# Performance work log

Measured on AMD Instinct MI355X. Metric: run time of the kernel, lower is better.

The kernel has to match this reference:

```python
import jax, jax.numpy as jnp
import numpy as np

N = 100000          # num nodes
E = 3200000         # num edges
H = 512             # hidden_dim
B = 512             # num graphs (batch.max()+1)
MAX_NODES = 500
TEMPERATURE = 1.0
LN_EPS = 1e-5
COS_EPS = 1e-8


def setup_inputs() -> dict:
    key = jax.random.key(0)
    ks = jax.random.split(key, 12)
    x_ggnn = jax.random.normal(ks[0], (N, H), dtype=jnp.float32)
    x_appnp = jax.random.normal(ks[1], (N, H), dtype=jnp.float32)
    edge_index = jax.random.randint(ks[2], (2, E), 0, N, dtype=jnp.int64)
    batch = jnp.sort(jax.random.randint(ks[3], (N,), 0, B, dtype=jnp.int64))
    gin = H * 2 + 4  # gate input dim = 1028
    def xavier(k, fan_in, fan_out, gain=1.0):
        lim = gain * np.sqrt(6.0 / (fan_in + fan_out))
        return jax.random.uniform(k, (fan_in, fan_out), jnp.float32, -lim, lim)
    W1 = xavier(ks[4], gin, H)
    b1 = jnp.zeros((H,), jnp.float32)
    ln_g = jnp.ones((H,), jnp.float32)
    ln_b = jnp.zeros((H,), jnp.float32)
    W2 = xavier(ks[5], H, H // 2)
    b2 = jnp.zeros((H // 2,), jnp.float32)
    W3 = xavier(ks[6], H // 2, 2, gain=0.1)
    b3 = jnp.zeros((2,), jnp.float32)  # init zeros per module
    return {"x_ggnn": x_ggnn, "x_appnp": x_appnp, "edge_index": edge_index,
            "batch": batch, "W1": W1, "b1": b1, "ln_g": ln_g, "ln_b": ln_b,
            "W2": W2, "b2": b2, "W3": W3, "b3": b3}


def _segment_mean(x, seg, num_seg, counts):
    s = jax.ops.segment_sum(x, seg, num_segments=num_seg)
    return s / counts[:, None]


def reference(x_ggnn, x_appnp, edge_index, batch, W1, b1, ln_g, ln_b, W2, b2, W3, b3):
    ones = jnp.ones((N,), jnp.float32)
    counts = jax.ops.segment_sum(ones, batch, num_segments=B)          # [B] nodes per graph
    safe_counts = jnp.maximum(counts, 1.0)
    # per-graph edge counts (edges with both endpoints in same graph)
    src_g = batch[edge_index[0]]
    dst_g = batch[edge_index[1]]
    same = (src_g == dst_g).astype(jnp.float32)
    n_edges = jax.ops.segment_sum(same, src_g, num_segments=B)          # [B]
    # pooled (segment mean) features
    pooled_ggnn = _segment_mean(x_ggnn, batch, B, safe_counts)          # [B,H]
    pooled_appnp = _segment_mean(x_appnp, batch, B, safe_counts)        # [B,H]
    # complexity features
    n_nodes = counts
    scale = jnp.log(n_nodes + 1.0) / np.log(MAX_NODES + 1.0)
    density = n_edges / (n_nodes * (n_nodes - 1.0) + 1e-8)
    avg_degree = n_edges / (n_nodes + 1e-8)
    avg_degree_norm = jnp.minimum(avg_degree / 10.0, 1.0)
    na = jnp.maximum(jnp.linalg.norm(pooled_ggnn, axis=1), COS_EPS)
    nb = jnp.maximum(jnp.linalg.norm(pooled_appnp, axis=1), COS_EPS)
    cos = jnp.sum(pooled_ggnn * pooled_appnp, axis=1) / (na * nb)
    divergence = (1.0 - cos) / 2.0
    complexity = jnp.stack([scale, density, avg_degree_norm, divergence], axis=1)  # [B,4]
    # gate MLP (dropout inactive at inference)
    g = jnp.concatenate([pooled_ggnn, pooled_appnp, complexity], axis=1)  # [B, 2H+4]
    h = g @ W1 + b1
    mu = jnp.mean(h, axis=-1, keepdims=True)
    var = jnp.mean((h - mu) ** 2, axis=-1, keepdims=True)
    h = (h - mu) / jnp.sqrt(var + LN_EPS) * ln_g + ln_b
    h = jax.nn.relu(h)
    h = jax.nn.relu(h @ W2 + b2)
    raw = h @ W3 + b3                                                    # [B,2]
    weights = jax.nn.softmax(raw / TEMPERATURE, axis=1)
    w_local = weights[:, 0]
    w_global = weights[:, 1]
    x_fused = w_local[batch][:, None] * x_ggnn + w_global[batch][:, None] * x_appnp
    return x_fused
```

## Files before the change

kernel.cpp:

```cpp
#include <hip/hip_runtime.h>
#include <math.h>

#define Nn 100000
#define Ee 3200000
#define Hh 512
#define Bb 512
#define GIN 1028

#define OFF_STARTS 0
#define OFF_NEDGE  4096
#define OFF_WL     8192
#define OFF_WG     10240
#define OFF_G      16384
#define OFF_HPART  (OFF_G + (size_t)Bb*GIN*4)
#define OFF_H      (OFF_HPART + (size_t)4*Bb*Hh*4)
#define OFF_HP2    (OFF_H + (size_t)Bb*Hh*4)

__global__ void k_starts(const int* __restrict__ batch, int* __restrict__ starts) {
    int t = threadIdx.x;
    for (int b = t; b <= Bb; b += blockDim.x) {
        int lo = 0, hi = Nn;
        while (lo < hi) { int mid = (lo + hi) >> 1; if (batch[mid] < b) lo = mid + 1; else hi = mid; }
        starts[b] = lo;
    }
}

__global__ void k_edges(const int* __restrict__ ei, const int* __restrict__ batch,
                        int* __restrict__ nedge) {
    int e = blockIdx.x * blockDim.x + threadIdx.x;
    if (e >= Ee) return;
    int s = ei[e], d = ei[Ee + e];
    int gs = batch[s], gd = batch[d];
    if (gs == gd) atomicAdd(&nedge[gs], 1);
}

__global__ __launch_bounds__(256) void k_pool(const float* __restrict__ xg, const float* __restrict__ xa,
                                              const int* __restrict__ starts, const int* __restrict__ nedge,
                                              float* __restrict__ g) {
    int b = blockIdx.x;
    int s = starts[b], e = starts[b + 1];
    int t = threadIdx.x;
    int arr = t >> 7, c4 = t & 127;
    const float4* base = (const float4*)(arr ? xa : xg);
    float4 acc = {0.f, 0.f, 0.f, 0.f};
    for (int i = s; i < e; ++i) {
        float4 v = base[(size_t)i * 128 + c4];
        acc.x += v.x; acc.y += v.y; acc.z += v.z; acc.w += v.w;
    }
    int cnt = e - s;
    float inv = 1.0f / (float)(cnt < 1 ? 1 : cnt);
    float4 m = {acc.x * inv, acc.y * inv, acc.z * inv, acc.w * inv};
    float* grow = g + (size_t)b * GIN;
    *(float4*)(grow + arr * Hh + c4 * 4) = m;

    __shared__ float4 sa[128];
    if (arr) sa[c4] = m;
    __syncthreads();
    float d3 = 0.f, ng = 0.f, na = 0.f;
    if (!arr) {
        float4 q = sa[c4];
        d3 = m.x * q.x + m.y * q.y + m.z * q.z + m.w * q.w;
        ng = m.x * m.x + m.y * m.y + m.z * m.z + m.w * m.w;
    } else {
        na = m.x * m.x + m.y * m.y + m.z * m.z + m.w * m.w;
    }
    for (int off = 32; off; off >>= 1) {
        d3 += __shfl_down(d3, off);
        ng += __shfl_down(ng, off);
        na += __shfl_down(na, off);
    }
    __shared__ float r[12];
    int wid = t >> 6, lane = t & 63;
    if (lane == 0) { r[wid * 3] = d3; r[wid * 3 + 1] = ng; r[wid * 3 + 2] = na; }
    __syncthreads();
    if (t == 0) {
        float D  = r[0] + r[3] + r[6] + r[9];
        float NG = r[1] + r[4] + r[7] + r[10];
        float NA = r[2] + r[5] + r[8] + r[11];
        float nag = fmaxf(sqrtf(NG), 1e-8f);
        float nab = fmaxf(sqrtf(NA), 1e-8f);
        float cosv = D / (nag * nab);
        float n  = (float)cnt;
        float ne = (float)nedge[b];
        grow[1024] = logf(n + 1.f) / logf(501.f);
        grow[1025] = ne / (n * (n - 1.f) + 1e-8f);
        grow[1026] = fminf(ne / (n + 1e-8f) * 0.1f, 1.f);
        grow[1027] = (1.f - cosv) * 0.5f;
    }
}

__global__ __launch_bounds__(256) void k_g1(const float* __restrict__ g, const float* __restrict__ W1,
                                            float* __restrict__ hp) {
    int tj = threadIdx.x & 15, tb = threadIdx.x >> 4;
    int j0 = blockIdx.x * 64 + tj * 4;
    int b0 = blockIdx.y * 64 + tb * 4;
    int kc = blockIdx.z;
    int k = kc * 257, kend = k + 257;
    const float* g0 = g + (size_t)b0 * GIN;
    const float* g1 = g0 + GIN;
    const float* g2 = g1 + GIN;
    const float* g3 = g2 + GIN;
    float4 a0 = {0,0,0,0}, a1 = a0, a2 = a0, a3 = a0;
    for (; k < kend; ++k) {
        float4 w = *(const float4*)(W1 + (size_t)k * Hh + j0);
        float x0 = g0[k], x1 = g1[k], x2 = g2[k], x3 = g3[k];
        a0.x += x0 * w.x; a0.y += x0 * w.y; a0.z += x0 * w.z; a0.w += x0 * w.w;
        a1.x += x1 * w.x; a1.y += x1 * w.y; a1.z += x1 * w.z; a1.w += x1 * w.w;
        a2.x += x2 * w.x; a2.y += x2 * w.y; a2.z += x2 * w.z; a2.w += x2 * w.w;
        a3.x += x3 * w.x; a3.y += x3 * w.y; a3.z += x3 * w.z; a3.w += x3 * w.w;
    }
    float* o = hp + ((size_t)kc * Bb + b0) * Hh + j0;
    *(float4*)(o)           = a0;
    *(float4*)(o + Hh)      = a1;
    *(float4*)(o + 2 * Hh)  = a2;
    *(float4*)(o + 3 * Hh)  = a3;
}

__global__ __launch_bounds__(128) void k_ln(const float* __restrict__ hp, const float* __restrict__ b1,
                                            const float* __restrict__ lng, const float* __restrict__ lnb,
                                            float* __restrict__ h) {
    int b = blockIdx.x, t = threadIdx.x;
    const float4* p0 = (const float4*)(hp + (size_t)b * Hh);
    const float4* p1 = (const float4*)(hp + ((size_t)Bb + b) * Hh);
    const float4* p2 = (const float4*)(hp + ((size_t)2 * Bb + b) * Hh);
    const float4* p3 = (const float4*)(hp + ((size_t)3 * Bb + b) * Hh);
    float4 v0 = p0[t], v1 = p1[t], v2 = p2[t], v3 = p3[t], bb = ((const float4*)b1)[t];
    float4 v = {v0.x + v1.x + v2.x + v3.x + bb.x,
                v0.y + v1.y + v2.y + v3.y + bb.y,
                v0.z + v1.z + v2.z + v3.z + bb.z,
                v0.w + v1.w + v2.w + v3.w + bb.w};
    float s  = v.x + v.y + v.z + v.w;
    float ss = v.x * v.x + v.y * v.y + v.z * v.z + v.w * v.w;
    for (int off = 32; off; off >>= 1) { s += __shfl_down(s, off); ss += __shfl_down(ss, off); }
    __shared__ float sh[4];
    __shared__ float mus, rs;
    int wid = t >> 6, lane = t & 63;
    if (lane == 0) { sh[wid * 2] = s; sh[wid * 2 + 1] = ss; }
    __syncthreads();
    if (t == 0) {
        float S = sh[0] + sh[2], SS = sh[1] + sh[3];
        float mu = S * (1.f / 512.f);
        float var = SS * (1.f / 512.f) - mu * mu;
        mus = mu; rs = rsqrtf(var + 1e-5f);
    }
    __syncthreads();
    float mu = mus, rstd = rs;
    float4 gg = ((const float4*)lng)[t], be = ((const float4*)lnb)[t];
    float4 o;
    o.x = fmaxf((v.x - mu) * rstd * gg.x + be.x, 0.f);
    o.y = fmaxf((v.y - mu) * rstd * gg.y + be.y, 0.f);
    o.z = fmaxf((v.z - mu) * rstd * gg.z + be.z, 0.f);
    o.w = fmaxf((v.w - mu) * rstd * gg.w + be.w, 0.f);
    ((float4*)(h + (size_t)b * Hh))[t] = o;
}

__global__ __launch_bounds__(256) void k_g2(const float* __restrict__ h, const float* __restrict__ W2,
                                            float* __restrict__ hp2) {
    int tj = threadIdx.x & 15, tb = threadIdx.x >> 4;
    int j0 = blockIdx.x * 64 + tj * 4;
    int b0 = blockIdx.y * 64 + tb * 4;
    int kc = blockIdx.z;
    int k = kc * 256, kend = k + 256;
    const float* h0 = h + (size_t)b0 * Hh;
    const float* h1 = h0 + Hh;
    const float* h2 = h1 + Hh;
    const float* h3 = h2 + Hh;
    float4 a0 = {0,0,0,0}, a1 = a0, a2 = a0, a3 = a0;
    for (; k < kend; ++k) {
        float4 w = *(const float4*)(W2 + (size_t)k * 256 + j0);
        float x0 = h0[k], x1 = h1[k], x2 = h2[k], x3 = h3[k];
        a0.x += x0 * w.x; a0.y += x0 * w.y; a0.z += x0 * w.z; a0.w += x0 * w.w;
        a1.x += x1 * w.x; a1.y += x1 * w.y; a1.z += x1 * w.z; a1.w += x1 * w.w;
        a2.x += x2 * w.x; a2.y += x2 * w.y; a2.z += x2 * w.z; a2.w += x2 * w.w;
        a3.x += x3 * w.x; a3.y += x3 * w.y; a3.z += x3 * w.z; a3.w += x3 * w.w;
    }
    float* o = hp2 + ((size_t)kc * Bb + b0) * 256 + j0;
    *(float4*)(o)          = a0;
    *(float4*)(o + 256)    = a1;
    *(float4*)(o + 512)    = a2;
    *(float4*)(o + 768)    = a3;
}

__global__ __launch_bounds__(64) void k_g3(const float* __restrict__ hp2, const float* __restrict__ b2,
                                           const float* __restrict__ W3, const float* __restrict__ b3,
                                           float* __restrict__ wl, float* __restrict__ wg) {
    int b = blockIdx.x, t = threadIdx.x;
    const float4* p0 = (const float4*)(hp2 + (size_t)b * 256);
    const float4* p1 = (const float4*)(hp2 + ((size_t)Bb + b) * 256);
    float4 v0 = p0[t], v1 = p1[t], bb = ((const float4*)b2)[t];
    float h0 = fmaxf(v0.x + v1.x + bb.x, 0.f);
    float h1 = fmaxf(v0.y + v1.y + bb.y, 0.f);
    float h2 = fmaxf(v0.z + v1.z + bb.z, 0.f);
    float h3 = fmaxf(v0.w + v1.w + bb.w, 0.f);
    int j0 = t * 4;
    float r0 = h0 * W3[j0 * 2]     + h1 * W3[(j0 + 1) * 2]     + h2 * W3[(j0 + 2) * 2]     + h3 * W3[(j0 + 3) * 2];
    float r1 = h0 * W3[j0 * 2 + 1] + h1 * W3[(j0 + 1) * 2 + 1] + h2 * W3[(j0 + 2) * 2 + 1] + h3 * W3[(j0 + 3) * 2 + 1];
    for (int off = 32; off; off >>= 1) { r0 += __shfl_down(r0, off); r1 += __shfl_down(r1, off); }
    if (t == 0) {
        float raw0 = r0 + b3[0], raw1 = r1 + b3[1];
        float mx = fmaxf(raw0, raw1);
        float e0 = expf(raw0 - mx), e1 = expf(raw1 - mx);
        float inv = 1.f / (e0 + e1);
        wl[b] = e0 * inv;
        wg[b] = e1 * inv;
    }
}

__global__ __launch_bounds__(256) void k_fuse(const float* __restrict__ xg, const float* __restrict__ xa,
                                              const int* __restrict__ batch, const float* __restrict__ wl,
                                              const float* __restrict__ wg, float* __restrict__ out) {
    size_t tid = (size_t)blockIdx.x * 256 + threadIdx.x;
    if (tid >= (size_t)Nn * (Hh / 4)) return;
    int i = (int)(tid >> 7);
    int b = batch[i];
    float l = wl[b], gl = wg[b];
    float4 a = ((const float4*)xg)[tid];
    float4 p = ((const float4*)xa)[tid];
    float4 o = {l * a.x + gl * p.x, l * a.y + gl * p.y, l * a.z + gl * p.z, l * a.w + gl * p.w};
    ((float4*)out)[tid] = o;
}

extern "C" void kernel_launch(void* const* d_in, const int* in_sizes, int n_in,
                              void* d_out, int out_size, void* d_ws, size_t ws_size,
                              hipStream_t stream) {
    const float* xg   = (const float*)d_in[0];
    const float* xa   = (const float*)d_in[1];
    const int*   ei   = (const int*)d_in[2];
    const int*   batch= (const int*)d_in[3];
    const float* W1   = (const float*)d_in[4];
    const float* b1   = (const float*)d_in[5];
    const float* lng  = (const float*)d_in[6];
    const float* lnb  = (const float*)d_in[7];
    const float* W2   = (const float*)d_in[8];
    const float* b2   = (const float*)d_in[9];
    const float* W3   = (const float*)d_in[10];
    const float* b3   = (const float*)d_in[11];
    float* out = (float*)d_out;

    char* ws = (char*)d_ws;
    int*   starts = (int*)(ws + OFF_STARTS);
    int*   nedge  = (int*)(ws + OFF_NEDGE);
    float* wl     = (float*)(ws + OFF_WL);
    float* wg     = (float*)(ws + OFF_WG);
    float* g      = (float*)(ws + OFF_G);
    float* hp     = (float*)(ws + OFF_HPART);
    float* h      = (float*)(ws + OFF_H);
    float* hp2    = (float*)(ws + OFF_HP2);

    hipMemsetAsync(nedge, 0, Bb * sizeof(int), stream);
    k_starts<<<1, 256, 0, stream>>>(batch, starts);
    k_edges<<<(Ee + 255) / 256, 256, 0, stream>>>(ei, batch, nedge);
    k_pool<<<Bb, 256, 0, stream>>>(xg, xa, starts, nedge, g);
    k_g1<<<dim3(8, 8, 4), 256, 0, stream>>>(g, W1, hp);
    k_ln<<<Bb, 128, 0, stream>>>(hp, b1, lng, lnb, h);
    k_g2<<<dim3(4, 8, 2), 256, 0, stream>>>(h, W2, hp2);
    k_g3<<<Bb, 64, 0, stream>>>(hp2, b2, W3, b3, wl, wg);
    k_fuse<<<(Nn * (Hh / 4) + 255) / 256, 256, 0, stream>>>(xg, xa, batch, wl, wg, out);
}
```

Before: 784.8 us.

## Split segment pooling across node chunks with unrolled accumulators and finalize pass

Segment-mean pooling now runs on a 2D grid where each graph's node range is split into PCH interleaved strides, giving four times as many blocks to pull the two 205 MB feature arrays. Each thread also keeps four independent float4 accumulators with four loads in flight per iteration to raise memory-level parallelism. A second small kernel sums the partials and does the normalization and cosine work that was previously in the single pool kernel. In exchange there is an extra launch plus writing and rereading a PCH x B x 1024 partial buffer, and the strided rows are less contiguous per block.

```diff
diff --git a/kernel.cpp b/kernel.cpp
--- a/kernel.cpp
+++ b/kernel.cpp
@@ -6,13 +6,15 @@
 #define Hh 512
 #define Bb 512
 #define GIN 1028
+#define PCH 4
 
 #define OFF_STARTS 0
 #define OFF_NEDGE  4096
 #define OFF_WL     8192
 #define OFF_WG     10240
 #define OFF_G      16384
-#define OFF_HPART  (OFF_G + (size_t)Bb*GIN*4)
+#define OFF_PP     (OFF_G + (size_t)Bb*GIN*4)
+#define OFF_HPART  (OFF_PP + (size_t)PCH*Bb*1024*4)
 #define OFF_H      (OFF_HPART + (size_t)4*Bb*Hh*4)
 #define OFF_HP2    (OFF_H + (size_t)Bb*Hh*4)
 
@@ -34,20 +36,49 @@
     if (gs == gd) atomicAdd(&nedge[gs], 1);
 }
 
-__global__ __launch_bounds__(256) void k_pool(const float* __restrict__ xg, const float* __restrict__ xa,
-                                              const int* __restrict__ starts, const int* __restrict__ nedge,
-                                              float* __restrict__ g) {
-    int b = blockIdx.x;
+__global__ __launch_bounds__(256) void k_pool_part(const float* __restrict__ xg, const float* __restrict__ xa,
+                                                   const int* __restrict__ starts, float* __restrict__ pp) {
+    int b = blockIdx.x, c = blockIdx.y;
     int s = starts[b], e = starts[b + 1];
     int t = threadIdx.x;
     int arr = t >> 7, c4 = t & 127;
     const float4* base = (const float4*)(arr ? xa : xg);
-    float4 acc = {0.f, 0.f, 0.f, 0.f};
-    for (int i = s; i < e; ++i) {
-        float4 v = base[(size_t)i * 128 + c4];
-        acc.x += v.x; acc.y += v.y; acc.z += v.z; acc.w += v.w;
-    }
+    float4 a0 = {0.f,0.f,0.f,0.f}, a1 = a0, a2 = a0, a3 = a0;
+    int i = s + c;
+    const float4* p = base + (size_t)i * 128 + c4;
+    for (; i + 3 * PCH < e; i += 4 * PCH, p += 4 * PCH * 128) {
+        float4 v0 = p[0];
+        float4 v1 = p[PCH * 128];
+        float4 v2 = p[2 * PCH * 128];
+        float4 v3 = p[3 * PCH * 128];
+        a0.x += v0.x; a0.y += v0.y; a0.z += v0.z; a0.w += v0.w;
+        a1.x += v1.x; a1.y += v1.y; a1.z += v1.z; a1.w += v1.w;
+        a2.x += v2.x; a2.y += v2.y; a2.z += v2.z; a2.w += v2.w;
+        a3.x += v3.x; a3.y += v3.y; a3.z += v3.z; a3.w += v3.w;
+    }
+    for (; i < e; i += PCH, p += PCH * 128) {
+        float4 v = p[0];
+        a0.x += v.x; a0.y += v.y; a0.z += v.z; a0.w += v.w;
+    }
+    float4 acc = {a0.x + a1.x + a2.x + a3.x,
+                  a0.y + a1.y + a2.y + a3.y,
+                  a0.z + a1.z + a2.z + a3.z,
+                  a0.w + a1.w + a2.w + a3.w};
+    ((float4*)(pp + ((size_t)(c * Bb + b)) * 1024))[t] = acc;
+}
+
+__global__ __launch_bounds__(256) void k_pool_fin(const float* __restrict__ pp, const int* __restrict__ starts,
+                                                  const int* __restrict__ nedge, float* __restrict__ g) {
+    int b = blockIdx.x, t = threadIdx.x;
+    int s = starts[b], e = starts[b + 1];
     int cnt = e - s;
+    int arr = t >> 7, c4 = t & 127;
+    float4 acc = {0.f,0.f,0.f,0.f};
+    #pragma unroll
+    for (int c = 0; c < PCH; ++c) {
+        float4 u = ((const float4*)(pp + ((size_t)(c * Bb + b)) * 1024))[t];
+        acc.x += u.x; acc.y += u.y; acc.z += u.z; acc.w += u.w;
+    }
     float inv = 1.0f / (float)(cnt < 1 ? 1 : cnt);
     float4 m = {acc.x * inv, acc.y * inv, acc.z * inv, acc.w * inv};
     float* grow = g + (size_t)b * GIN;
@@ -243,6 +274,7 @@
     float* wl     = (float*)(ws + OFF_WL);
     float* wg     = (float*)(ws + OFF_WG);
     float* g      = (float*)(ws + OFF_G);
+    float* pp     = (float*)(ws + OFF_PP);
     float* hp     = (float*)(ws + OFF_HPART);
     float* h      = (float*)(ws + OFF_H);
     float* hp2    = (float*)(ws + OFF_HP2);
@@ -250,7 +282,8 @@
     hipMemsetAsync(nedge, 0, Bb * sizeof(int), stream);
     k_starts<<<1, 256, 0, stream>>>(batch, starts);
     k_edges<<<(Ee + 255) / 256, 256, 0, stream>>>(ei, batch, nedge);
-    k_pool<<<Bb, 256, 0, stream>>>(xg, xa, starts, nedge, g);
+    k_pool_part<<<dim3(Bb, PCH), 256, 0, stream>>>(xg, xa, starts, pp);
+    k_pool_fin<<<Bb, 256, 0, stream>>>(pp, starts, nedge, g);
     k_g1<<<dim3(8, 8, 4), 256, 0, stream>>>(g, W1, hp);
     k_ln<<<Bb, 128, 0, stream>>>(hp, b1, lng, lnb, h);
     k_g2<<<dim3(4, 8, 2), 256, 0, stream>>>(h, W2, hp2);
```

Result: faster. 764.0 us (-2.6%).
